# Kernel optimization log

Hardware: AMD Instinct MI355X
Metric: run time of the kernel (lower is better)

## Reference

```python
import jax, jax.numpy as jnp
import numpy as np

B, S, D, H = 2, 2048, 1024, 16
DK = D // H


def setup_inputs() -> dict:
    key = jax.random.key(0)
    ks = jax.random.split(key, 9)
    def xavier(k, shape):
        fan_in, fan_out = shape[1], shape[0]
        lim = jnp.sqrt(6.0 / (fan_in + fan_out))
        return jax.random.uniform(k, shape, jnp.float32, -lim, lim)
    x = jax.random.normal(ks[0], (B, S, D), jnp.float32)
    mask = jnp.ones((B, 1, S), jnp.int32)
    Wq = xavier(ks[1], (D, D)); bq = jnp.zeros((D,), jnp.float32)
    Wk = xavier(ks[2], (D, D)); bk = jnp.zeros((D,), jnp.float32)
    Wv = xavier(ks[3], (D, D)); bv = jnp.zeros((D,), jnp.float32)
    Wo = xavier(ks[4], (D, D)); bo = jnp.zeros((D,), jnp.float32)
    return {"x": x, "mask": mask, "Wq": Wq, "bq": bq, "Wk": Wk, "bk": bk,
            "Wv": Wv, "bv": bv, "Wo": Wo, "bo": bo}


def reference(x, mask, Wq, bq, Wk, bk, Wv, bv, Wo, bo):
    # Linear layers use torch convention y = x @ W.T + b
    q = (x @ Wq.T + bq).reshape(B, S, H, DK).transpose(0, 2, 1, 3)  # [B,H,S,DK]
    k = (x @ Wk.T + bk).reshape(B, S, H, DK).transpose(0, 2, 1, 3)
    v = (x @ Wv.T + bv).reshape(B, S, H, DK).transpose(0, 2, 1, 3)
    scores = jnp.einsum('bhqd,bhkd->bhqk', q, k) / jnp.sqrt(jnp.float32(DK))
    m = mask[:, None, :, :]  # unsqueeze(1): broadcast over heads -> [B,1,1,S]
    scores = jnp.where(m == 0, jnp.float32(-1e9), scores)
    p = jax.nn.softmax(scores, axis=-1)  # dropout p=0.0 -> identity
    ctx = jnp.einsum('bhqk,bhkd->bhqd', p, v)
    ctx = ctx.transpose(0, 2, 1, 3).reshape(B, S, D)
    return ctx @ Wo.T + bo
```

## Files before the change

### kernel.cpp

```cpp
#include <hip/hip_runtime.h>
#include <hip/hip_bf16.h>
#include <math.h>

#define Bn 2
#define Sn 2048
#define Dn 1024
#define Hn 16
#define DKn 64
#define BHS (Bn * Hn * Sn)

using fragb  = __attribute__((ext_vector_type(8))) short;
using frag16 = __attribute__((ext_vector_type(8))) _Float16;
using f4     = __attribute__((ext_vector_type(4))) float;

__device__ __forceinline__ short f2bf(float f) {
    union { float f; unsigned u; } v; v.f = f;
    unsigned r = v.u + 0x7FFF + ((v.u >> 16) & 1);
    return (short)(r >> 16);
}
__device__ __forceinline__ unsigned short f2h(float f) {
    _Float16 h = (_Float16)f;
    unsigned short s; __builtin_memcpy(&s, &h, 2); return s;
}

#define GLOAD(gptr, lptr)                                                     \
    __builtin_amdgcn_global_load_lds(                                         \
        (const __attribute__((address_space(1))) unsigned int*)(const void*)(gptr), \
        (__attribute__((address_space(3))) unsigned int*)(void*)(lptr), 16, 0, 0)

#define NX (Bn * Sn * Dn)
#define NW (Dn * Dn)
#define NF4 ((NX + 4 * NW) / 4)

__global__ __launch_bounds__(256) void prep(
    const float* __restrict__ x,  const float* __restrict__ Wq,
    const float* __restrict__ Wk, const float* __restrict__ Wv,
    const float* __restrict__ Wo, const int* __restrict__ mask,
    short* __restrict__ xh,
    short* __restrict__ Wqh, short* __restrict__ Wkh,
    short* __restrict__ Wvh, short* __restrict__ Woh,
    short* __restrict__ mfb)
{
    int i = blockIdx.x * 256 + threadIdx.x;
    if (i < NF4) {
        int e = i << 2;
        const float* src; short* dst; int j;
        if (e < NX)               { src = x;  dst = xh;  j = e; }
        else if (e < NX + NW)     { src = Wq; dst = Wqh; j = e - NX; }
        else if (e < NX + 2 * NW) { src = Wk; dst = Wkh; j = e - NX - NW; }
        else if (e < NX + 3 * NW) { src = Wv; dst = Wvh; j = e - NX - 2 * NW; }
        else                      { src = Wo; dst = Woh; j = e - NX - 3 * NW; }
        float4 v = *(const float4*)(src + j);
        ushort4 o;
        o.x = f2h(v.x); o.y = f2h(v.y); o.z = f2h(v.z); o.w = f2h(v.w);
        *(ushort4*)(dst + j) = o;
    } else {
        int j = (i - NF4) << 2;
        if (j < Bn * Sn) {
            int4 m = *(const int4*)(mask + j);
            ushort4 o;
            o.x = m.x ? 0x3F80 : 0; o.y = m.y ? 0x3F80 : 0;
            o.z = m.z ? 0x3F80 : 0; o.w = m.w ? 0x3F80 : 0;
            *(ushort4*)(mfb + j) = o;
        }
    }
}

__global__ __launch_bounds__(256) void gemm_qkv(
    const short* __restrict__ A,
    const short* __restrict__ W0, const float* __restrict__ b0,
    const short* __restrict__ W1, const float* __restrict__ b1,
    const short* __restrict__ W2, const float* __restrict__ b2,
    const int* __restrict__ mask,
    short* __restrict__ Qb, short* __restrict__ Kb, short* __restrict__ Vtb)
{
    __shared__ __align__(16) short As[128 * 32];
    __shared__ __align__(16) short Bs[128 * 32];

    const int tid  = threadIdx.x;
    const int wave = tid >> 6;
    const int lane = tid & 63;
    const int quad = lane >> 4;
    const int l16  = lane & 15;
    const int wm   = wave >> 1;
    const int wn   = wave & 1;

    const int m0   = blockIdx.y * 128;
    const int n0   = blockIdx.x * 128;
    const int widx = n0 >> 10;
    const int nl0  = n0 & 1023;

    const short* Wp   = widx == 0 ? W0 : (widx == 1 ? W1 : W2);
    const float* bias = widx == 0 ? b0 : (widx == 1 ? b1 : b2);

    f4 acc[4][4];
    #pragma unroll
    for (int i = 0; i < 4; i++)
        #pragma unroll
        for (int j = 0; j < 4; j++) {
            acc[i][j][0] = 0.f; acc[i][j][1] = 0.f;
            acc[i][j][2] = 0.f; acc[i][j][3] = 0.f;
        }

    const int K  = Dn;
    const int r0 = tid >> 2;
    const int r1 = (tid + 256) >> 2;
    const int sc = ((tid & 3) ^ ((tid >> 3) & 3)) * 8;
    const short* Ar0 = A  + (size_t)(m0  + r0) * K + sc;
    const short* Ar1 = A  + (size_t)(m0  + r1) * K + sc;
    const short* Br0 = Wp + (size_t)(nl0 + r0) * K + sc;
    const short* Br1 = Wp + (size_t)(nl0 + r1) * K + sc;

    const int cA = (quad ^ ((l16 >> 1) & 3)) * 8;

    for (int k0 = 0; k0 < K; k0 += 32) {
        __syncthreads();
        GLOAD(Ar0 + k0, &As[(wave * 64) * 8]);
        GLOAD(Ar1 + k0, &As[(256 + wave * 64) * 8]);
        GLOAD(Br0 + k0, &Bs[(wave * 64) * 8]);
        GLOAD(Br1 + k0, &Bs[(256 + wave * 64) * 8]);
        __syncthreads();

        frag16 a[4], b[4];
        #pragma unroll
        for (int mi = 0; mi < 4; mi++)
            a[mi] = *(const frag16*)&As[(wm * 64 + mi * 16 + l16) * 32 + cA];
        #pragma unroll
        for (int ni = 0; ni < 4; ni++)
            b[ni] = *(const frag16*)&Bs[(wn * 64 + ni * 16 + l16) * 32 + cA];
        #pragma unroll
        for (int mi = 0; mi < 4; mi++)
            #pragma unroll
            for (int ni = 0; ni < 4; ni++)
                acc[mi][ni] = __builtin_amdgcn_mfma_f32_16x16x32_f16(
                    a[mi], b[ni], acc[mi][ni], 0, 0, 0);
    }

    const float QSCALE = 0.125f * 1.44269504088896340736f;

    #pragma unroll
    for (int mi = 0; mi < 4; mi++) {
        #pragma unroll
        for (int ni = 0; ni < 4; ni++) {
            int nl = nl0 + wn * 64 + ni * 16 + l16;
            float bv = bias[nl];
            #pragma unroll
            for (int r = 0; r < 4; r++) {
                int m = m0 + wm * 64 + mi * 16 + quad * 4 + r;
                float v = acc[mi][ni][r] + bv;
                int b  = m >> 11, s = m & (Sn - 1);
                int h  = nl >> 6, dk = nl & 63;
                if (widx == 0)
                    Qb[((size_t)(b * Hn + h) * Sn + s) * DKn + dk] = f2bf(v * QSCALE);
                else if (widx == 1)
                    Kb[((size_t)(b * Hn + h) * Sn + s) * DKn + dk] = f2bf(v);
                else {
                    float mv = (float)mask[b * Sn + s];
                    Vtb[((size_t)(b * Hn + h) * DKn + dk) * Sn + s] = f2bf(v * mv);
                }
            }
        }
    }
}

__global__ __launch_bounds__(256) void gemm_out(
    const short* __restrict__ A, const short* __restrict__ Wp,
    const float* __restrict__ bias, float* __restrict__ outf)
{
    __shared__ __align__(16) short As[64 * 32];
    __shared__ __align__(16) short Bs[128 * 32];

    const int tid  = threadIdx.x;
    const int wave = tid >> 6;
    const int lane = tid & 63;
    const int quad = lane >> 4;
    const int l16  = lane & 15;
    const int wm   = wave >> 1;
    const int wn   = wave & 1;

    const int m0 = blockIdx.y * 64;
    const int n0 = blockIdx.x * 128;

    f4 acc[2][4];
    #pragma unroll
    for (int i = 0; i < 2; i++)
        #pragma unroll
        for (int j = 0; j < 4; j++) {
            acc[i][j][0] = 0.f; acc[i][j][1] = 0.f;
            acc[i][j][2] = 0.f; acc[i][j][3] = 0.f;
        }

    const int K  = Dn;
    const int r0 = tid >> 2;
    const int r1 = (tid + 256) >> 2;
    const int sc = ((tid & 3) ^ ((tid >> 3) & 3)) * 8;
    const short* Ar0 = A  + (size_t)(m0 + r0) * K + sc;
    const short* Br0 = Wp + (size_t)(n0 + r0) * K + sc;
    const short* Br1 = Wp + (size_t)(n0 + r1) * K + sc;

    const int cA = (quad ^ ((l16 >> 1) & 3)) * 8;

    for (int k0 = 0; k0 < K; k0 += 32) {
        __syncthreads();
        GLOAD(Ar0 + k0, &As[(wave * 64) * 8]);
        GLOAD(Br0 + k0, &Bs[(wave * 64) * 8]);
        GLOAD(Br1 + k0, &Bs[(256 + wave * 64) * 8]);
        __syncthreads();

        frag16 a[2], b[4];
        #pragma unroll
        for (int mi = 0; mi < 2; mi++)
            a[mi] = *(const frag16*)&As[(wm * 32 + mi * 16 + l16) * 32 + cA];
        #pragma unroll
        for (int ni = 0; ni < 4; ni++)
            b[ni] = *(const frag16*)&Bs[(wn * 64 + ni * 16 + l16) * 32 + cA];
        #pragma unroll
        for (int mi = 0; mi < 2; mi++)
            #pragma unroll
            for (int ni = 0; ni < 4; ni++)
                acc[mi][ni] = __builtin_amdgcn_mfma_f32_16x16x32_f16(
                    a[mi], b[ni], acc[mi][ni], 0, 0, 0);
    }

    #pragma unroll
    for (int mi = 0; mi < 2; mi++) {
        #pragma unroll
        for (int ni = 0; ni < 4; ni++) {
            int nl = n0 + wn * 64 + ni * 16 + l16;
            float bv = bias[nl];
            #pragma unroll
            for (int r = 0; r < 4; r++) {
                int m = m0 + wm * 32 + mi * 16 + quad * 4 + r;
                outf[(size_t)m * Dn + nl] = acc[mi][ni][r] + bv;
            }
        }
    }
}

#define LP  72

__global__ __launch_bounds__(256) void attn_mfma(
    const short* __restrict__ Qb, const short* __restrict__ Kb,
    const short* __restrict__ Vtb, const short* __restrict__ mfb,
    short* __restrict__ Ch)
{
    __shared__ __align__(16) short Ks[2][64 * 64];
    __shared__ __align__(16) short Vs[2][64 * 64];
    __shared__ short Ps[4][32 * LP];
    __shared__ __align__(16) short mfs[128];

    const int tid  = threadIdx.x;
    const int wave = tid >> 6;
    const int lane = tid & 63;
    const int quad = lane >> 4;
    const int l16  = lane & 15;

    const int x   = blockIdx.x;
    const int bhh = (x & 7) + ((x >> 7) << 3);
    const int qt  = (x >> 3) & 15;
    const int b   = bhh >> 4;
    const int h   = bhh & 15;

    fragb qf[2][2];
    #pragma unroll
    for (int w = 0; w < 2; w++) {
        int qrow = qt * 128 + wave * 32 + w * 16 + l16;
        const short* qptr = Qb + ((size_t)bhh * Sn + qrow) * DKn + quad * 8;
        qf[w][0] = *(const fragb*)(qptr);
        qf[w][1] = *(const fragb*)(qptr + 32);
    }

    f4 ctx[2][4];
    #pragma unroll
    for (int w = 0; w < 2; w++)
        #pragma unroll
        for (int dt = 0; dt < 4; dt++) {
            ctx[w][dt][0] = 0.f; ctx[w][dt][1] = 0.f;
            ctx[w][dt][2] = 0.f; ctx[w][dt][3] = 0.f;
        }
    f4 lacc[2];
    lacc[0][0] = 0.f; lacc[0][1] = 0.f; lacc[0][2] = 0.f; lacc[0][3] = 0.f;
    lacc[1] = lacc[0];

    const int lr = lane >> 3;
    const int sc = ((lane & 7) ^ lr) * 8;
    const short* Kg = Kb  + (size_t)bhh * Sn * DKn;
    const short* Vg = Vtb + (size_t)bhh * DKn * Sn;
    const short* mg = mfb + (size_t)b * Sn;

    const short* Ksrc = Kg + (size_t)(wave * 16 + lr) * DKn + sc;
    const short* Vsrc = Vg + (size_t)(wave * 16 + lr) * Sn + sc;

    const int c0 = ((quad ^ (l16 & 7)) * 8);

    for (int r = 0; r < 16; r++) {
        __syncthreads();
        GLOAD(Ksrc + (size_t)(2 * r) * 4096,               &Ks[0][(wave * 16) * 64]);
        GLOAD(Ksrc + (size_t)(2 * r) * 4096 + 8 * DKn,     &Ks[0][(wave * 16 + 8) * 64]);
        GLOAD(Ksrc + (size_t)(2 * r + 1) * 4096,           &Ks[1][(wave * 16) * 64]);
        GLOAD(Ksrc + (size_t)(2 * r + 1) * 4096 + 8 * DKn, &Ks[1][(wave * 16 + 8) * 64]);
        GLOAD(Vsrc + (size_t)(2 * r) * 64,                 &Vs[0][(wave * 16) * 64]);
        GLOAD(Vsrc + (size_t)(2 * r) * 64 + 8 * Sn,        &Vs[0][(wave * 16 + 8) * 64]);
        GLOAD(Vsrc + (size_t)(2 * r + 1) * 64,             &Vs[1][(wave * 16) * 64]);
        GLOAD(Vsrc + (size_t)(2 * r + 1) * 64 + 8 * Sn,    &Vs[1][(wave * 16 + 8) * 64]);
        if (tid < 16)
            *(uint4*)&mfs[tid * 8] = *(const uint4*)(mg + r * 128 + tid * 8);
        __syncthreads();

        #pragma unroll
        for (int hs = 0; hs < 2; hs++) {
            #pragma unroll
            for (int t = 0; t < 4; t++) {
                fragb k0 = *(const fragb*)&Ks[hs][(t * 16 + l16) * 64 + c0];
                fragb k1 = *(const fragb*)&Ks[hs][(t * 16 + l16) * 64 + (c0 ^ 32)];
                #pragma unroll
                for (int w = 0; w < 2; w++) {
                    f4 a; a[0] = 0.f; a[1] = 0.f; a[2] = 0.f; a[3] = 0.f;
                    __builtin_amdgcn_s_setprio(1);
                    a = __builtin_amdgcn_mfma_f32_16x16x32_bf16(k0, qf[w][0], a, 0, 0, 0);
                    a = __builtin_amdgcn_mfma_f32_16x16x32_bf16(k1, qf[w][1], a, 0, 0, 0);
                    __builtin_amdgcn_s_setprio(0);
                    unsigned u0 = __float_as_uint(__builtin_amdgcn_exp2f(a[0]));
                    unsigned u1 = __float_as_uint(__builtin_amdgcn_exp2f(a[1]));
                    unsigned u2 = __float_as_uint(__builtin_amdgcn_exp2f(a[2]));
                    unsigned u3 = __float_as_uint(__builtin_amdgcn_exp2f(a[3]));
                    uint2 pw;
                    pw.x = __builtin_amdgcn_perm(u1, u0, 0x07060302u);
                    pw.y = __builtin_amdgcn_perm(u3, u2, 0x07060302u);
                    *(uint2*)&Ps[wave][(w * 16 + l16) * LP + 16 * t + quad * 4] = pw;
                }
            }

            fragb p[2][2];
            #pragma unroll
            for (int w = 0; w < 2; w++) {
                p[w][0] = *(const fragb*)&Ps[wave][(w * 16 + l16) * LP + quad * 8];
                p[w][1] = *(const fragb*)&Ps[wave][(w * 16 + l16) * LP + quad * 8 + 32];
            }
            fragb m0 = *(const fragb*)&mfs[hs * 64 + quad * 8];
            fragb m1 = *(const fragb*)&mfs[hs * 64 + quad * 8 + 32];
            __builtin_amdgcn_s_setprio(1);
            #pragma unroll
            for (int w = 0; w < 2; w++) {
                lacc[w] = __builtin_amdgcn_mfma_f32_16x16x32_bf16(p[w][0], m0, lacc[w], 0, 0, 0);
                lacc[w] = __builtin_amdgcn_mfma_f32_16x16x32_bf16(p[w][1], m1, lacc[w], 0, 0, 0);
            }
            #pragma unroll
            for (int dt = 0; dt < 4; dt++) {
                fragb v0 = *(const fragb*)&Vs[hs][(dt * 16 + l16) * 64 + c0];
                fragb v1 = *(const fragb*)&Vs[hs][(dt * 16 + l16) * 64 + (c0 ^ 32)];
                #pragma unroll
                for (int w = 0; w < 2; w++) {
                    ctx[w][dt] = __builtin_amdgcn_mfma_f32_16x16x32_bf16(p[w][0], v0, ctx[w][dt], 0, 0, 0);
                    ctx[w][dt] = __builtin_amdgcn_mfma_f32_16x16x32_bf16(p[w][1], v1, ctx[w][dt], 0, 0, 0);
                }
            }
            __builtin_amdgcn_s_setprio(0);
        }
    }

    #pragma unroll
    for (int w = 0; w < 2; w++)
        #pragma unroll
        for (int r = 0; r < 4; r++) {
            int row = qt * 128 + wave * 32 + w * 16 + quad * 4 + r;
            float inv = 1.f / lacc[w][r];
            #pragma unroll
            for (int dt = 0; dt < 4; dt++)
                Ch[((size_t)(b * Sn + row)) * Dn + h * DKn + dt * 16 + l16] =
                    f2h(ctx[w][dt][r] * inv);
        }
}

extern "C" void kernel_launch(void* const* d_in, const int* in_sizes, int n_in,
                              void* d_out, int out_size, void* d_ws, size_t ws_size,
                              hipStream_t stream) {
    const float* x    = (const float*)d_in[0];
    const int*   mask = (const int*)d_in[1];
    const float* Wq   = (const float*)d_in[2];
    const float* bq   = (const float*)d_in[3];
    const float* Wk   = (const float*)d_in[4];
    const float* bk   = (const float*)d_in[5];
    const float* Wv   = (const float*)d_in[6];
    const float* bv   = (const float*)d_in[7];
    const float* Wo   = (const float*)d_in[8];
    const float* bo   = (const float*)d_in[9];
    float* out = (float*)d_out;

    char* ws = (char*)d_ws;
    const size_t MB = 1024u * 1024u;
    short* xh    = (short*)(ws + 0 * MB);
    short* Wqh   = (short*)(ws + 8 * MB);
    short* Wkh   = (short*)(ws + 10 * MB);
    short* Wvh   = (short*)(ws + 12 * MB);
    short* Qb    = (short*)(ws + 16 * MB);
    short* Kb    = (short*)(ws + 24 * MB);
    short* Vtb   = (short*)(ws + 32 * MB);
    short* Woh   = (short*)(ws + 56 * MB);
    short* mfb   = (short*)(ws + 59 * MB);
    short* Ch    = (short*)(ws + 60 * MB);

    const int PRE = NF4 + (Bn * Sn) / 4;
    prep<<<(PRE + 255) / 256, 256, 0, stream>>>(
        x, Wq, Wk, Wv, Wo, mask, xh, Wqh, Wkh, Wvh, Woh, mfb);

    gemm_qkv<<<dim3(24, 32), 256, 0, stream>>>(
        xh, Wqh, bq, Wkh, bk, Wvh, bv, mask, Qb, Kb, Vtb);

    attn_mfma<<<dim3(Bn * Hn * (Sn / 128)), 256, 0, stream>>>(
        Qb, Kb, Vtb, mfb, Ch);

    gemm_out<<<dim3(8, 64), 256, 0, stream>>>(Ch, Woh, bo, out);
}
```

Before: 203.4 us.

## Prefetch next K/V tile into registers while computing current tile

Replaces the direct global-to-LDS loads of each K/V/mask tile with a register-staged software pipeline. The next iteration's tiles are loaded into registers after the barrier, overlapping global latency with the MFMA and softmax work, and are written to LDS at the start of the next iteration. This adds 8+ uint4 registers per thread, which can lower occupancy, and gives up the direct-to-LDS load path.

```diff
diff --git a/kernel.cpp b/kernel.cpp
--- a/kernel.cpp
+++ b/kernel.cpp
@@ -291,21 +291,50 @@
     const short* Ksrc = Kg + (size_t)(wave * 16 + lr) * DKn + sc;
     const short* Vsrc = Vg + (size_t)(wave * 16 + lr) * Sn + sc;
 
+    short* dK0a = &Ks[0][(wave * 16) * 64 + lane * 8];
+    short* dK0b = &Ks[0][(wave * 16 + 8) * 64 + lane * 8];
+    short* dK1a = &Ks[1][(wave * 16) * 64 + lane * 8];
+    short* dK1b = &Ks[1][(wave * 16 + 8) * 64 + lane * 8];
+    short* dV0a = &Vs[0][(wave * 16) * 64 + lane * 8];
+    short* dV0b = &Vs[0][(wave * 16 + 8) * 64 + lane * 8];
+    short* dV1a = &Vs[1][(wave * 16) * 64 + lane * 8];
+    short* dV1b = &Vs[1][(wave * 16 + 8) * 64 + lane * 8];
+
     const int c0 = ((quad ^ (l16 & 7)) * 8);
 
+    uint4 rg[8];
+    uint4 mreg;
+
+#define LOADREGS(r) do {                                                      \
+    rg[0] = *(const uint4*)(Ksrc + (size_t)(2 * (r)) * 4096);                 \
+    rg[1] = *(const uint4*)(Ksrc + (size_t)(2 * (r)) * 4096 + 8 * DKn);       \
+    rg[2] = *(const uint4*)(Ksrc + (size_t)(2 * (r) + 1) * 4096);             \
+    rg[3] = *(const uint4*)(Ksrc + (size_t)(2 * (r) + 1) * 4096 + 8 * DKn);   \
+    rg[4] = *(const uint4*)(Vsrc + (size_t)(2 * (r)) * 64);                   \
+    rg[5] = *(const uint4*)(Vsrc + (size_t)(2 * (r)) * 64 + 8 * Sn);          \
+    rg[6] = *(const uint4*)(Vsrc + (size_t)(2 * (r) + 1) * 64);               \
+    rg[7] = *(const uint4*)(Vsrc + (size_t)(2 * (r) + 1) * 64 + 8 * Sn);      \
+    if (tid < 16) mreg = *(const uint4*)(mg + (r) * 128 + tid * 8);           \
+} while (0)
+
+#define WRITELDS() do {                                                       \
+    *(uint4*)dK0a = rg[0];                                                    \
+    *(uint4*)dK0b = rg[1];                                                    \
+    *(uint4*)dK1a = rg[2];                                                    \
+    *(uint4*)dK1b = rg[3];                                                    \
+    *(uint4*)dV0a = rg[4];                                                    \
+    *(uint4*)dV0b = rg[5];                                                    \
+    *(uint4*)dV1a = rg[6];                                                    \
+    *(uint4*)dV1b = rg[7];                                                    \
+    if (tid < 16) *(uint4*)&mfs[tid * 8] = mreg;                              \
+} while (0)
+
+    LOADREGS(0);
     for (int r = 0; r < 16; r++) {
         __syncthreads();
-        GLOAD(Ksrc + (size_t)(2 * r) * 4096,               &Ks[0][(wave * 16) * 64]);
-        GLOAD(Ksrc + (size_t)(2 * r) * 4096 + 8 * DKn,     &Ks[0][(wave * 16 + 8) * 64]);
-        GLOAD(Ksrc + (size_t)(2 * r + 1) * 4096,           &Ks[1][(wave * 16) * 64]);
-        GLOAD(Ksrc + (size_t)(2 * r + 1) * 4096 + 8 * DKn, &Ks[1][(wave * 16 + 8) * 64]);
-        GLOAD(Vsrc + (size_t)(2 * r) * 64,                 &Vs[0][(wave * 16) * 64]);
-        GLOAD(Vsrc + (size_t)(2 * r) * 64 + 8 * Sn,        &Vs[0][(wave * 16 + 8) * 64]);
-        GLOAD(Vsrc + (size_t)(2 * r + 1) * 64,             &Vs[1][(wave * 16) * 64]);
-        GLOAD(Vsrc + (size_t)(2 * r + 1) * 64 + 8 * Sn,    &Vs[1][(wave * 16 + 8) * 64]);
-        if (tid < 16)
-            *(uint4*)&mfs[tid * 8] = *(const uint4*)(mg + r * 128 + tid * 8);
-        __syncthreads();
+        WRITELDS();
+        __syncthreads();
+        if (r < 15) LOADREGS(r + 1);
 
         #pragma unroll
         for (int hs = 0; hs < 2; hs++) {
```

After: 250.4 us. +23.1%, slower.
